# Optimization experiments

Hardware: AMD Instinct MI355X
Metric: run time of the kernel (lower is better)

The kernel has to match this reference:

```python
import jax, jax.numpy as jnp
import numpy as np
from jax import lax

B, C1, C2, OUT, H, W = 8, 256, 128, 256, 64, 64
MID = max(C1, C2)
D = max(MID // 8, 4)

def conv1x1(x, w, b=None):
    # x: [B,C,H,W], w: [O,C]
    y = jnp.einsum('bchw,oc->bohw', x, w)
    if b is not None:
        y = y + b[None, :, None, None]
    return y

def dwconv3x3(x, w, b):
    # depthwise 3x3, padding=1; w: [C,1,3,3]
    y = lax.conv_general_dilated(x, w, (1, 1), 'SAME',
                                 dimension_numbers=('NCHW', 'OIHW', 'NCHW'),
                                 feature_group_count=x.shape[1])
    return y + b[None, :, None, None]

def setup_inputs() -> dict:
    key = jax.random.key(0)
    ks = jax.random.split(key, 16)
    def w1x1(k, o, i):
        return jax.random.normal(k, (o, i), jnp.float32) * np.sqrt(2.0 / o)
    def wdw(k, c):
        return jax.random.normal(k, (c, 1, 3, 3), jnp.float32) * np.sqrt(2.0 / (9 * c))
    z = lambda c: jnp.zeros((c,), jnp.float32)
    return {
        'x1': jax.random.normal(ks[0], (B, C1, H, W), jnp.float32),
        'x2': jax.random.normal(ks[1], (B, C2, H, W), jnp.float32),
        'conv_r_w': w1x1(ks[2], MID, C1), 'conv_r_b': z(MID),
        'conv_n_w': w1x1(ks[3], MID, C2), 'conv_n_b': z(MID),
        'mlp_w1': w1x1(ks[4], D, MID),
        'mlp_w2': w1x1(ks[5], 2 * MID, D),
        'pq_w': w1x1(ks[6], MID, MID), 'pq_b': z(MID),
        'dq_w': wdw(ks[7], MID), 'dq_b': z(MID),
        'pk_w': w1x1(ks[8], MID, MID), 'pk_b': z(MID),
        'dk_w': wdw(ks[9], MID), 'dk_b': z(MID),
        'pv_w': w1x1(ks[10], MID, MID), 'pv_b': z(MID),
        'dv_w': wdw(ks[11], MID), 'dv_b': z(MID),
        'out_w': w1x1(ks[12], OUT, MID), 'out_b': z(OUT),
        'alpha': jnp.float32(1.0),
        'lambd': jnp.float32(0.5),
        'beta': jnp.float32(0.5),
    }

def reference(x1, x2, conv_r_w, conv_r_b, conv_n_w, conv_n_b, mlp_w1, mlp_w2,
              pq_w, pq_b, dq_w, dq_b, pk_w, pk_b, dk_w, dk_b,
              pv_w, pv_b, dv_w, dv_b, out_w, out_b, alpha, lambd, beta):
    FR = conv1x1(x1, conv_r_w, conv_r_b)          # [B,C,H,W]
    FN = conv1x1(x2, conv_n_w, conv_n_b)          # [B,C,H,W]
    stack = jnp.stack([FR, FN], axis=1)           # [B,2,C,H,W]
    feats_sum = FR + FN
    pooled = feats_sum.mean(axis=(2, 3))          # [B,C] (adaptive avg pool 1x1)
    h = jax.nn.relu(jnp.einsum('bc,dc->bd', pooled, mlp_w1))
    a = jnp.einsum('bd,ed->be', h, mlp_w2).reshape(B, 2, MID)
    attn = jax.nn.softmax(a, axis=1)              # softmax over the 2 branches
    Fw = jnp.einsum('bkchw,bkc->bchw', stack, attn)
    Q = dwconv3x3(conv1x1(Fw, pq_w, pq_b), dq_w, dq_b)
    K = dwconv3x3(conv1x1(Fw, pk_w, pk_b), dk_w, dk_b)
    V = dwconv3x3(conv1x1(Fw, pv_w, pv_b), dv_w, dv_b)
    FQ = jnp.fft.fft2(Q.astype(jnp.float32), axes=(-2, -1))   # complex64 [B,C,H,W]
    FK = jnp.fft.fft2(K.astype(jnp.float32), axes=(-2, -1))
    elem = (FQ * FK).reshape(B, MID, H * W)                    # [B,C,HW]
    FQf = FQ.reshape(B, MID, H * W)
    FKf = FK.reshape(B, MID, H * W)
    attn_matrix = jnp.einsum('bcn,bdn->bcd', FQf, FKf)         # complex [B,C,C]
    attn_w = jax.nn.softmax(jnp.abs(attn_matrix) / alpha, axis=-1)
    attn_wc = attn_w.astype(jnp.complex64)
    F_CFR = jnp.einsum('bcd,bdn->bcn', attn_wc, elem).reshape(B, MID, H, W)
    cfr = jnp.real(jnp.fft.ifft2(F_CFR, axes=(-2, -1))).astype(Q.dtype)
    F_DFR = V - lambd * V * cfr
    freq_out = Q * cfr + F_DFR
    output = beta * freq_out + (1.0 - beta) * Fw
    return conv1x1(output, out_w, out_b)
```

## Files before the change

kernel.cpp:

```cpp
#include <hip/hip_runtime.h>
#include <math.h>

#ifndef M_PI
#define M_PI 3.14159265358979323846
#endif

typedef unsigned int u32;

constexpr int  NB   = 8;
constexpr int  CH   = 256;
constexpr long HW   = 4096;
constexpr long SLOT = (long)NB * CH * HW;
constexpr int  SPLITK = 8;
constexpr long ST   = (long)CH * HW;

__device__ __forceinline__ float rne_hi(float x) {
  unsigned u = __float_as_uint(x);
  unsigned r = (u + 0x7FFFu + ((u >> 16) & 1u)) & 0xFFFF0000u;
  return __uint_as_float(r);
}
__device__ __forceinline__ u32 packf(float x) {
  const float h = rne_hi(x);
  const float l = x - h;
  return (__float_as_uint(h) & 0xFFFF0000u) | (__float_as_uint(l) >> 16);
}
__device__ __forceinline__ float unpackf(u32 u) {
  return __uint_as_float(u & 0xFFFF0000u) + __uint_as_float(u << 16);
}
__device__ __forceinline__ unsigned bfpair(float x, float y) {
  return (__float_as_uint(x) >> 16) | (__float_as_uint(y) & 0xFFFF0000u);
}

typedef short bf16x8 __attribute__((ext_vector_type(8)));
typedef float f32x4  __attribute__((ext_vector_type(4)));

__global__ __launch_bounds__(256)
void cvt_kernel(const float* __restrict__ src, u32* __restrict__ dst, int n4)
{
  const int i = blockIdx.x * 256 + threadIdx.x;
  if (i < n4) {
    const float4 v = ((const float4*)src)[i];
    uint4 o;
    o.x = packf(v.x); o.y = packf(v.y); o.z = packf(v.z); o.w = packf(v.w);
    ((uint4*)dst)[i] = o;
  }
}

template<bool BPACKED, int EPI>
__global__ __launch_bounds__(256)
void gemm_mfma(const u32* __restrict__ A, const void* __restrict__ Bv,
               void* __restrict__ Cv, const float* __restrict__ bias,
               int K, long aStride, long bStride, long cStride,
               const u32* __restrict__ qb, const u32* __restrict__ vb,
               const u32* __restrict__ fwb,
               const float* __restrict__ lambd, const float* __restrict__ beta)
{
  constexpr int N = 4096;
  __shared__ __align__(16) unsigned short sAh[128 * 48];
  __shared__ __align__(16) unsigned short sAl[128 * 48];
  __shared__ __align__(16) unsigned short sBh[128 * 48];
  __shared__ __align__(16) unsigned short sBl[128 * 48];

  const int tid = threadIdx.x;
  const int b   = blockIdx.z;
  const int m0  = blockIdx.y * 128;
  const int n0  = blockIdx.x * 128;
  const u32* Ab = A + (long)b * aStride;

  const int ar = tid >> 1;
  const int ak = (tid & 1) * 16;
  const int aBase = ar * 48 + ak;
  const int bn = tid & 127;
  const int bk = (tid >> 7) * 16;
  const int bBase = bn * 48 + bk;

  const int wv = tid >> 6, lane = tid & 63;
  const int wy = wv >> 1, wx = wv & 1;
  const int quad = lane >> 4, l15 = lane & 15;

  f32x4 acc[4][4];
#pragma unroll
  for (int i = 0; i < 4; ++i)
#pragma unroll
    for (int j = 0; j < 4; ++j) acc[i][j] = (f32x4){0.f, 0.f, 0.f, 0.f};

  u32   ra[16];
  u32   rbu[16];
  float rbf[16];
  {
    const u32* ap = Ab + (long)(m0 + ar) * K + ak;
#pragma unroll
    for (int i = 0; i < 4; ++i) {
      const uint4 t = *(const uint4*)(ap + i * 4);
      ra[4*i] = t.x; ra[4*i+1] = t.y; ra[4*i+2] = t.z; ra[4*i+3] = t.w;
    }
    if (BPACKED) {
      const u32* bp = (const u32*)Bv + (long)b * bStride + (long)bk * N + n0 + bn;
#pragma unroll
      for (int i = 0; i < 16; ++i) rbu[i] = bp[(long)i * N];
    } else {
      const float* bp = (const float*)Bv + (long)b * bStride + (long)bk * N + n0 + bn;
#pragma unroll
      for (int i = 0; i < 16; ++i) rbf[i] = bp[(long)i * N];
    }
  }

  for (int kt = 0; kt < K; kt += 32) {
    {
      u32 hi[8], lo[8];
#pragma unroll
      for (int e = 0; e < 8; ++e) {
        const u32 u0 = ra[2*e], u1 = ra[2*e+1];
        hi[e] = (u0 >> 16) | (u1 & 0xFFFF0000u);
        lo[e] = (u0 & 0xFFFFu) | (u1 << 16);
      }
      *(uint4*)&sAh[aBase]     = make_uint4(hi[0], hi[1], hi[2], hi[3]);
      *(uint4*)&sAh[aBase + 8] = make_uint4(hi[4], hi[5], hi[6], hi[7]);
      *(uint4*)&sAl[aBase]     = make_uint4(lo[0], lo[1], lo[2], lo[3]);
      *(uint4*)&sAl[aBase + 8] = make_uint4(lo[4], lo[5], lo[6], lo[7]);
    }
    if (BPACKED) {
      u32 hi[8], lo[8];
#pragma unroll
      for (int e = 0; e < 8; ++e) {
        const u32 u0 = rbu[2*e], u1 = rbu[2*e+1];
        hi[e] = (u0 >> 16) | (u1 & 0xFFFF0000u);
        lo[e] = (u0 & 0xFFFFu) | (u1 << 16);
      }
      *(uint4*)&sBh[bBase]     = make_uint4(hi[0], hi[1], hi[2], hi[3]);
      *(uint4*)&sBh[bBase + 8] = make_uint4(hi[4], hi[5], hi[6], hi[7]);
      *(uint4*)&sBl[bBase]     = make_uint4(lo[0], lo[1], lo[2], lo[3]);
      *(uint4*)&sBl[bBase + 8] = make_uint4(lo[4], lo[5], lo[6], lo[7]);
    } else {
      float h[16], l[16];
#pragma unroll
      for (int e = 0; e < 16; ++e) { h[e] = rne_hi(rbf[e]); l[e] = rbf[e] - h[e]; }
      *(uint4*)&sBh[bBase]     = make_uint4(bfpair(h[0],h[1]), bfpair(h[2],h[3]),
                                            bfpair(h[4],h[5]), bfpair(h[6],h[7]));
      *(uint4*)&sBh[bBase + 8] = make_uint4(bfpair(h[8],h[9]), bfpair(h[10],h[11]),
                                            bfpair(h[12],h[13]), bfpair(h[14],h[15]));
      *(uint4*)&sBl[bBase]     = make_uint4(bfpair(l[0],l[1]), bfpair(l[2],l[3]),
                                            bfpair(l[4],l[5]), bfpair(l[6],l[7]));
      *(uint4*)&sBl[bBase + 8] = make_uint4(bfpair(l[8],l[9]), bfpair(l[10],l[11]),
                                            bfpair(l[12],l[13]), bfpair(l[14],l[15]));
    }
    __syncthreads();

    if (kt + 32 < K) {
      const u32* ap = Ab + (long)(m0 + ar) * K + kt + 32 + ak;
#pragma unroll
      for (int i = 0; i < 4; ++i) {
        const uint4 t = *(const uint4*)(ap + i * 4);
        ra[4*i] = t.x; ra[4*i+1] = t.y; ra[4*i+2] = t.z; ra[4*i+3] = t.w;
      }
      if (BPACKED) {
        const u32* bp = (const u32*)Bv + (long)b * bStride + (long)(kt + 32 + bk) * N + n0 + bn;
#pragma unroll
        for (int i = 0; i < 16; ++i) rbu[i] = bp[(long)i * N];
      } else {
        const float* bp = (const float*)Bv + (long)b * bStride + (long)(kt + 32 + bk) * N + n0 + bn;
#pragma unroll
        for (int i = 0; i < 16; ++i) rbf[i] = bp[(long)i * N];
      }
    }

    bf16x8 ah[4], al[4];
#pragma unroll
    for (int i = 0; i < 4; ++i) {
      const int idx = (wy * 64 + i * 16 + l15) * 48 + quad * 8;
      ah[i] = *(const bf16x8*)&sAh[idx];
      al[i] = *(const bf16x8*)&sAl[idx];
    }
#pragma unroll
    for (int j = 0; j < 4; ++j) {
      const int idx = (wx * 64 + j * 16 + l15) * 48 + quad * 8;
      const bf16x8 bh = *(const bf16x8*)&sBh[idx];
      const bf16x8 bl = *(const bf16x8*)&sBl[idx];
#pragma unroll
      for (int i = 0; i < 4; ++i) {
        acc[i][j] = __builtin_amdgcn_mfma_f32_16x16x32_bf16(ah[i], bh, acc[i][j], 0, 0, 0);
        acc[i][j] = __builtin_amdgcn_mfma_f32_16x16x32_bf16(ah[i], bl, acc[i][j], 0, 0, 0);
        acc[i][j] = __builtin_amdgcn_mfma_f32_16x16x32_bf16(al[i], bh, acc[i][j], 0, 0, 0);
      }
    }
    __syncthreads();
  }

  if (EPI == 0) {
    float* Cb = (float*)Cv + (long)b * cStride;
#pragma unroll
    for (int i = 0; i < 4; ++i)
#pragma unroll
      for (int r = 0; r < 4; ++r) {
        const int row = m0 + wy * 64 + i * 16 + quad * 4 + r;
        const float bb = bias ? bias[row] : 0.f;
#pragma unroll
        for (int j = 0; j < 4; ++j) {
          const int col = n0 + wx * 64 + j * 16 + l15;
          Cb[(long)row * N + col] = acc[i][j][r] + bb;
        }
      }
  } else if (EPI == 1) {
    u32* Cb = (u32*)Cv + (long)b * cStride;
#pragma unroll
    for (int i = 0; i < 4; ++i)
#pragma unroll
      for (int r = 0; r < 4; ++r) {
        const int row = m0 + wy * 64 + i * 16 + quad * 4 + r;
        const float bb = bias ? bias[row] : 0.f;
#pragma unroll
        for (int j = 0; j < 4; ++j) {
          const int col = n0 + wx * 64 + j * 16 + l15;
          Cb[(long)row * N + col] = packf(acc[i][j][r] + bb);
        }
      }
  } else {
    u32* Cb = (u32*)Cv + (long)b * cStride;
    const float lam = lambd[0], bet = beta[0];
#pragma unroll
    for (int i = 0; i < 4; ++i)
#pragma unroll
      for (int r = 0; r < 4; ++r) {
        const int row = m0 + wy * 64 + i * 16 + quad * 4 + r;
#pragma unroll
        for (int j = 0; j < 4; ++j) {
          const int col = n0 + wx * 64 + j * 16 + l15;
          const long off = (long)row * N + col;
          const long gi  = (long)b * cStride + off;
          const float q = unpackf(qb[gi]);
          const float v = unpackf(vb[gi]);
          const float f = unpackf(fwb[gi]);
          Cb[off] = packf(bet * (acc[i][j][r] * (q - lam * v) + v) + (1.f - bet) * f);
        }
      }
  }
}

__global__ __launch_bounds__(256)
void gemm_logits(const u32* __restrict__ Q, const u32* __restrict__ Kr,
                 float* __restrict__ Lp)
{
  __shared__ __align__(16) unsigned short sAh[128 * 48];
  __shared__ __align__(16) unsigned short sAl[128 * 48];
  __shared__ __align__(16) unsigned short sBh[128 * 48];
  __shared__ __align__(16) unsigned short sBl[128 * 48];

  const int tid = threadIdx.x;
  const int bz  = blockIdx.z;
  const int b   = bz >> 3, sp = bz & 7;
  const int m0  = blockIdx.y * 128;
  const int n0  = blockIdx.x * 128;
  const long k0b = (long)sp * 512;

  const int ar = tid >> 1;
  const int ak = (tid & 1) * 16;
  const int aBase = ar * 48 + ak;

  const int wv = tid >> 6, lane = tid & 63;
  const int wy = wv >> 1, wx = wv & 1;
  const int quad = lane >> 4, l15 = lane & 15;

  f32x4 acc[4][4];
#pragma unroll
  for (int i = 0; i < 4; ++i)
#pragma unroll
    for (int j = 0; j < 4; ++j) acc[i][j] = (f32x4){0.f, 0.f, 0.f, 0.f};

  const u32* Abase = Q  + (long)b * ST + (long)(m0 + ar) * 4096 + k0b + ak;
  const u32* Bbase = Kr + (long)b * ST + (long)(n0 + ar) * 4096 + k0b + ak;

  u32 ra[16], rb[16];
#pragma unroll
  for (int i = 0; i < 4; ++i) {
    uint4 t = *(const uint4*)(Abase + i * 4);
    ra[4*i] = t.x; ra[4*i+1] = t.y; ra[4*i+2] = t.z; ra[4*i+3] = t.w;
    t = *(const uint4*)(Bbase + i * 4);
    rb[4*i] = t.x; rb[4*i+1] = t.y; rb[4*i+2] = t.z; rb[4*i+3] = t.w;
  }

  for (int kt = 0; kt < 512; kt += 32) {
    {
      u32 hi[8], lo[8];
#pragma unroll
      for (int e = 0; e < 8; ++e) {
        const u32 u0 = ra[2*e], u1 = ra[2*e+1];
        hi[e] = (u0 >> 16) | (u1 & 0xFFFF0000u);
        lo[e] = (u0 & 0xFFFFu) | (u1 << 16);
      }
      *(uint4*)&sAh[aBase]     = make_uint4(hi[0], hi[1], hi[2], hi[3]);
      *(uint4*)&sAh[aBase + 8] = make_uint4(hi[4], hi[5], hi[6], hi[7]);
      *(uint4*)&sAl[aBase]     = make_uint4(lo[0], lo[1], lo[2], lo[3]);
      *(uint4*)&sAl[aBase + 8] = make_uint4(lo[4], lo[5], lo[6], lo[7]);
#pragma unroll
      for (int e = 0; e < 8; ++e) {
        const u32 u0 = rb[2*e], u1 = rb[2*e+1];
        hi[e] = (u0 >> 16) | (u1 & 0xFFFF0000u);
        lo[e] = (u0 & 0xFFFFu) | (u1 << 16);
      }
      *(uint4*)&sBh[aBase]     = make_uint4(hi[0], hi[1], hi[2], hi[3]);
      *(uint4*)&sBh[aBase + 8] = make_uint4(hi[4], hi[5], hi[6], hi[7]);
      *(uint4*)&sBl[aBase]     = make_uint4(lo[0], lo[1], lo[2], lo[3]);
      *(uint4*)&sBl[aBase + 8] = make_uint4(lo[4], lo[5], lo[6], lo[7]);
    }
    __syncthreads();

    if (kt + 32 < 512) {
#pragma unroll
      for (int i = 0; i < 4; ++i) {
        uint4 t = *(const uint4*)(Abase + kt + 32 + i * 4);
        ra[4*i] = t.x; ra[4*i+1] = t.y; ra[4*i+2] = t.z; ra[4*i+3] = t.w;
        t = *(const uint4*)(Bbase + kt + 32 + i * 4);
        rb[4*i] = t.x; rb[4*i+1] = t.y; rb[4*i+2] = t.z; rb[4*i+3] = t.w;
      }
    }

    bf16x8 ah[4], al[4];
#pragma unroll
    for (int i = 0; i < 4; ++i) {
      const int idx = (wy * 64 + i * 16 + l15) * 48 + quad * 8;
      ah[i] = *(const bf16x8*)&sAh[idx];
      al[i] = *(const bf16x8*)&sAl[idx];
    }
#pragma unroll
    for (int j = 0; j < 4; ++j) {
      const int idx = (wx * 64 + j * 16 + l15) * 48 + quad * 8;
      const bf16x8 bh = *(const bf16x8*)&sBh[idx];
      const bf16x8 bl = *(const bf16x8*)&sBl[idx];
#pragma unroll
      for (int i = 0; i < 4; ++i) {
        acc[i][j] = __builtin_amdgcn_mfma_f32_16x16x32_bf16(ah[i], bh, acc[i][j], 0, 0, 0);
        acc[i][j] = __builtin_amdgcn_mfma_f32_16x16x32_bf16(ah[i], bl, acc[i][j], 0, 0, 0);
        acc[i][j] = __builtin_amdgcn_mfma_f32_16x16x32_bf16(al[i], bh, acc[i][j], 0, 0, 0);
      }
    }
    __syncthreads();
  }

  float* Lb = Lp + (long)bz * 65536;
#pragma unroll
  for (int i = 0; i < 4; ++i)
#pragma unroll
    for (int r = 0; r < 4; ++r) {
      const int row = m0 + wy * 64 + i * 16 + quad * 4 + r;
#pragma unroll
      for (int j = 0; j < 4; ++j) {
        const int col = n0 + wx * 64 + j * 16 + l15;
        Lb[(long)row * 256 + col] = acc[i][j][r];
      }
    }
}

__global__ __launch_bounds__(256)
void pool_kernel(const u32* __restrict__ FR, const u32* __restrict__ FN,
                 float* __restrict__ pooled)
{
  __shared__ float red[256];
  const int bc = blockIdx.x, tid = threadIdx.x;
  const uint4* a = (const uint4*)(FR + (long)bc * HW);
  const uint4* b = (const uint4*)(FN + (long)bc * HW);
  float s = 0.f;
  for (int v = tid; v < 1024; v += 256) {
    const uint4 x = a[v];
    s += unpackf(x.x) + unpackf(x.y) + unpackf(x.z) + unpackf(x.w);
    const uint4 y = b[v];
    s += unpackf(y.x) + unpackf(y.y) + unpackf(y.z) + unpackf(y.w);
  }
  red[tid] = s; __syncthreads();
  for (int o = 128; o > 0; o >>= 1) {
    if (tid < o) red[tid] += red[tid + o];
    __syncthreads();
  }
  if (tid == 0) pooled[bc] = red[0] * (1.f / 4096.f);
}

__global__ __launch_bounds__(256)
void attn2_kernel(const float* __restrict__ pooled, const float* __restrict__ w1,
                  const float* __restrict__ w2, float* __restrict__ attn2)
{
  __shared__ float ps[256];
  __shared__ float hs[32];
  const int b = blockIdx.x, tid = threadIdx.x;
  ps[tid] = pooled[b * 256 + tid];
  __syncthreads();
  if (tid < 32) {
    float a = 0.f;
    for (int c = 0; c < 256; ++c) a += ps[c] * w1[tid * 256 + c];
    hs[tid] = fmaxf(a, 0.f);
  }
  __syncthreads();
  float a0 = 0.f, a1 = 0.f;
  for (int d = 0; d < 32; ++d) {
    const float h = hs[d];
    a0 += h * w2[tid * 32 + d];
    a1 += h * w2[(256 + tid) * 32 + d];
  }
  const float m  = fmaxf(a0, a1);
  const float e0 = expf(a0 - m), e1 = expf(a1 - m);
  const float inv = 1.f / (e0 + e1);
  attn2[b * 512 + tid]       = e0 * inv;
  attn2[b * 512 + 256 + tid] = e1 * inv;
}

__global__ __launch_bounds__(256)
void fw_kernel(const u32* __restrict__ FR, const u32* __restrict__ FN,
               const float* __restrict__ attn2, u32* __restrict__ FW)
{
  const int b = blockIdx.z, c = blockIdx.y;
  const float a0 = attn2[b * 512 + c];
  const float a1 = attn2[b * 512 + 256 + c];
  const long base4 = ((long)b * 256 + c) * 1024;
  const int i = blockIdx.x * 256 + threadIdx.x;
  const uint4 r = ((const uint4*)FR)[base4 + i];
  const uint4 n = ((const uint4*)FN)[base4 + i];
  uint4 o;
  o.x = packf(a0 * unpackf(r.x) + a1 * unpackf(n.x));
  o.y = packf(a0 * unpackf(r.y) + a1 * unpackf(n.y));
  o.z = packf(a0 * unpackf(r.z) + a1 * unpackf(n.z));
  o.w = packf(a0 * unpackf(r.w) + a1 * unpackf(n.w));
  ((uint4*)FW)[base4 + i] = o;
}

__global__ __launch_bounds__(256)
void dw_kernel(const u32* __restrict__ in, const float* __restrict__ w,
               const float* __restrict__ bias, u32* __restrict__ out,
               u32* __restrict__ out_rev)
{
  __shared__ float img[66][66];
  const int bc = blockIdx.x, tid = threadIdx.x;
  const int c = bc & 255;
  for (int v = tid; v < 66 * 66; v += 256) ((float*)img)[v] = 0.f;
  __syncthreads();
  const uint4* in4 = (const uint4*)(in + (long)bc * HW);
  for (int v = tid; v < 1024; v += 256) {
    const uint4 x = in4[v];
    const int r = v >> 4, c0 = ((v & 15) << 2) + 1;
    img[r + 1][c0 + 0] = unpackf(x.x);
    img[r + 1][c0 + 1] = unpackf(x.y);
    img[r + 1][c0 + 2] = unpackf(x.z);
    img[r + 1][c0 + 3] = unpackf(x.w);
  }
  float wr[9];
#pragma unroll
  for (int j = 0; j < 9; ++j) wr[j] = w[c * 9 + j];
  const float bb = bias[c];
  __syncthreads();
  for (int p = tid; p < 4096; p += 256) {
    const int y = p >> 6, x = p & 63;
    float s = bb;
#pragma unroll
    for (int ky = 0; ky < 3; ++ky)
#pragma unroll
      for (int kx = 0; kx < 3; ++kx)
        s = fmaf(wr[ky * 3 + kx], img[y + ky][x + kx], s);
    const u32 u = packf(s);
    out[(long)bc * HW + p] = u;
    if (out_rev)
      out_rev[(long)bc * HW + (((64 - y) & 63) << 6) + ((64 - x) & 63)] = u;
  }
}

#define SWA(r, c) (((r) << 6) | ((c) ^ (r)))
#define REV6(x)   ((((x) & 3) << 4) | ((x) & 12) | ((x) >> 4))

__device__ __forceinline__ float2 cmul(float2 a, float2 w) {
  return make_float2(a.x * w.x - a.y * w.y, a.x * w.y + a.y * w.x);
}
__device__ __forceinline__ float2 cmulc(float2 a, float2 w) {
  return make_float2(a.x * w.x + a.y * w.y, a.y * w.x - a.x * w.y);
}

__global__ __launch_bounds__(256, 4)
void sconv_kernel(const u32* __restrict__ Qg, const u32* __restrict__ Kg,
                  u32* __restrict__ Sg)
{
  __shared__ float Re[4096];
  __shared__ float Im[4096];
  __shared__ float2 twt[64];
  const int tid = threadIdx.x;
  const long base = (long)blockIdx.x * 4096;
  if (tid < 64) {
    float sn, cs;
    __sincosf(-2.f * (float)M_PI * (float)tid * (1.f / 64.f), &sn, &cs);
    twt[tid] = make_float2(cs, sn);
  }
  const uint4* Q4 = (const uint4*)(Qg + base);
  const uint4* K4 = (const uint4*)(Kg + base);
#pragma unroll
  for (int i = 0; i < 4; ++i) {
    const int v = tid + 256 * i;
    const uint4 q = Q4[v], k = K4[v];
    const int r = v >> 4, w = v & 15;
    const int R  = REV6(r);
    const int cb = ((w & 3) << 2) | (w >> 2);
    Re[SWA(R, cb)]      = unpackf(q.x);  Im[SWA(R, cb)]      = unpackf(k.x);
    Re[SWA(R, cb + 16)] = unpackf(q.y);  Im[SWA(R, cb + 16)] = unpackf(k.y);
    Re[SWA(R, cb + 32)] = unpackf(q.z);  Im[SWA(R, cb + 32)] = unpackf(k.z);
    Re[SWA(R, cb + 48)] = unpackf(q.w);  Im[SWA(R, cb + 48)] = unpackf(k.w);
  }
  __syncthreads();

  const int lane = tid & 63;
  const int kb   = tid >> 6;

  for (int pass = 0; pass < 2; ++pass) {
    for (int s = 0; s < 3; ++s) {
      const int h  = 1 << (2 * s);
      const int us = 16 >> (2 * s);
#pragma unroll
      for (int q = 0; q < 4; ++q) {
        const int k = kb + 4 * q;
        const int j = k & (h - 1);
        const int g = k >> (2 * s);
        const int bse = g * 4 * h + j;
        const int p0 = bse, p1 = bse + h, p2 = bse + 2 * h, p3 = bse + 3 * h;
        const int a0 = pass ? SWA(p0, lane) : SWA(lane, p0);
        const int a1 = pass ? SWA(p1, lane) : SWA(lane, p1);
        const int a2 = pass ? SWA(p2, lane) : SWA(lane, p2);
        const int a3 = pass ? SWA(p3, lane) : SWA(lane, p3);
        float2 x0 = make_float2(Re[a0], Im[a0]);
        float2 x1 = make_float2(Re[a1], Im[a1]);
        float2 x2 = make_float2(Re[a2], Im[a2]);
        float2 x3 = make_float2(Re[a3], Im[a3]);
        const int e = j * us;
        x1 = cmul(x1, twt[e & 63]);
        x2 = cmul(x2, twt[(2 * e) & 63]);
        x3 = cmul(x3, twt[(3 * e) & 63]);
        const float2 t0 = make_float2(x0.x + x2.x, x0.y + x2.y);
        const float2 t1 = make_float2(x0.x - x2.x, x0.y - x2.y);
        const float2 t2 = make_float2(x1.x + x3.x, x1.y + x3.y);
        const float2 t3 = make_float2(x1.x - x3.x, x1.y - x3.y);
        Re[a0] = t0.x + t2.x;  Im[a0] = t0.y + t2.y;
        Re[a2] = t0.x - t2.x;  Im[a2] = t0.y - t2.y;
        Re[a1] = t1.x + t3.y;  Im[a1] = t1.y - t3.x;
        Re[a3] = t1.x - t3.y;  Im[a3] = t1.y + t3.x;
      }
      __syncthreads();
    }
  }

  float2 pv[16];
#pragma unroll
  for (int i = 0; i < 16; ++i) {
    const int n = tid + 256 * i;
    const int u = n >> 6, vv = n & 63;
    const int u2 = (64 - u) & 63, v2 = (64 - vv) & 63;
    const int az = SWA(u, vv), am = SWA(u2, v2);
    const float zr = Re[az], zi = Im[az];
    const float mr = Re[am], mi = Im[am];
    const float dre = zr * zr - zi * zi - mr * mr + mi * mi;
    const float dim = 2.f * (zr * zi + mr * mi);
    pv[i] = make_float2(0.25f * dim, -0.25f * dre);
  }
  __syncthreads();
#pragma unroll
  for (int i = 0; i < 16; ++i) {
    const int n = tid + 256 * i;
    const int az = SWA(n >> 6, n & 63);
    Re[az] = pv[i].x;
    Im[az] = pv[i].y;
  }
  __syncthreads();

  for (int pass = 0; pass < 2; ++pass) {
    for (int s = 2; s >= 0; --s) {
      const int h  = 1 << (2 * s);
      const int us = 16 >> (2 * s);
#pragma unroll
      for (int q = 0; q < 4; ++q) {
        const int k = kb + 4 * q;
        const int j = k & (h - 1);
        const int g = k >> (2 * s);
        const int bse = g * 4 * h + j;
        const int p0 = bse, p1 = bse + h, p2 = bse + 2 * h, p3 = bse + 3 * h;
        const int a0 = pass ? SWA(lane, p0) : SWA(p0, lane);
        const int a1 = pass ? SWA(lane, p1) : SWA(p1, lane);
        const int a2 = pass ? SWA(lane, p2) : SWA(p2, lane);
        const int a3 = pass ? SWA(lane, p3) : SWA(p3, lane);
        const float2 x0 = make_float2(Re[a0], Im[a0]);
        const float2 x1 = make_float2(Re[a1], Im[a1]);
        const float2 x2 = make_float2(Re[a2], Im[a2]);
        const float2 x3 = make_float2(Re[a3], Im[a3]);
        const float2 t0 = make_float2(x0.x + x2.x, x0.y + x2.y);
        const float2 t1 = make_float2(x0.x - x2.x, x0.y - x2.y);
        const float2 t2 = make_float2(x1.x + x3.x, x1.y + x3.y);
        const float2 t3 = make_float2(x1.x - x3.x, x1.y - x3.y);
        const float2 y0 = make_float2(t0.x + t2.x, t0.y + t2.y);
        float2 y2 = make_float2(t0.x - t2.x, t0.y - t2.y);
        float2 y1 = make_float2(t1.x - t3.y, t1.y + t3.x);
        float2 y3 = make_float2(t1.x + t3.y, t1.y - t3.x);
        const int e = j * us;
        y1 = cmulc(y1, twt[e & 63]);
        y2 = cmulc(y2, twt[(2 * e) & 63]);
        y3 = cmulc(y3, twt[(3 * e) & 63]);
        Re[a0] = y0.x;  Im[a0] = y0.y;
        Re[a1] = y1.x;  Im[a1] = y1.y;
        Re[a2] = y2.x;  Im[a2] = y2.y;
        Re[a3] = y3.x;  Im[a3] = y3.y;
      }
      __syncthreads();
    }
  }

  uint4* S4 = (uint4*)(Sg + base);
#pragma unroll
  for (int i = 0; i < 4; ++i) {
    const int v = tid + 256 * i;
    const int y = v >> 4, w = v & 15;
    const int Rr = REV6(y);
    const int cb = ((w & 3) << 2) | (w >> 2);
    uint4 o;
    o.x = packf(Re[SWA(Rr, cb)]      * (1.f / 4096.f));
    o.y = packf(Re[SWA(Rr, cb + 16)] * (1.f / 4096.f));
    o.z = packf(Re[SWA(Rr, cb + 32)] * (1.f / 4096.f));
    o.w = packf(Re[SWA(Rr, cb + 48)] * (1.f / 4096.f));
    S4[v] = o;
  }
}

__global__ __launch_bounds__(256)
void softmax_kernel(const float* __restrict__ Lp, u32* __restrict__ L,
                    const float* __restrict__ alpha)
{
  __shared__ float red[256];
  const int row = blockIdx.x, tid = threadIdx.x;
  const int b = row >> 8, c = row & 255;
  const float sc = 4096.f / alpha[0];
  float acc = 0.f;
#pragma unroll
  for (int s = 0; s < SPLITK; ++s)
    acc += Lp[((long)(b * SPLITK + s) * 65536) + (long)c * 256 + tid];
  const float v = fabsf(acc) * sc;
  red[tid] = v; __syncthreads();
  for (int o = 128; o > 0; o >>= 1) {
    if (tid < o) red[tid] = fmaxf(red[tid], red[tid + o]);
    __syncthreads();
  }
  const float mx = red[0];
  __syncthreads();
  const float e = expf(v - mx);
  red[tid] = e; __syncthreads();
  for (int o = 128; o > 0; o >>= 1) {
    if (tid < o) red[tid] += red[tid + o];
    __syncthreads();
  }
  L[(long)row * 256 + tid] = packf(e / red[0]);
}

extern "C" void kernel_launch(void* const* d_in, const int* in_sizes, int n_in,
                              void* d_out, int out_size, void* d_ws, size_t ws_size,
                              hipStream_t stream)
{
  const float* x1       = (const float*)d_in[0];
  const float* x2       = (const float*)d_in[1];
  const float* conv_r_w = (const float*)d_in[2];
  const float* conv_r_b = (const float*)d_in[3];
  const float* conv_n_w = (const float*)d_in[4];
  const float* conv_n_b = (const float*)d_in[5];
  const float* mlp_w1   = (const float*)d_in[6];
  const float* mlp_w2   = (const float*)d_in[7];
  const float* pq_w     = (const float*)d_in[8];
  const float* pq_b     = (const float*)d_in[9];
  const float* dq_w     = (const float*)d_in[10];
  const float* dq_b     = (const float*)d_in[11];
  const float* pk_w     = (const float*)d_in[12];
  const float* pk_b     = (const float*)d_in[13];
  const float* dk_w     = (const float*)d_in[14];
  const float* dk_b     = (const float*)d_in[15];
  const float* pv_w     = (const float*)d_in[16];
  const float* pv_b     = (const float*)d_in[17];
  const float* dv_w     = (const float*)d_in[18];
  const float* dv_b     = (const float*)d_in[19];
  const float* out_w    = (const float*)d_in[20];
  const float* out_b    = (const float*)d_in[21];
  const float* alpha    = (const float*)d_in[22];
  const float* lambd    = (const float*)d_in[23];
  const float* beta     = (const float*)d_in[24];

  u32* s = (u32*)d_ws;
  u32* S0 = s;
  u32* S1 = s + SLOT;
  u32* S2 = s + 2 * SLOT;
  u32* S3 = s + 3 * SLOT;
  u32* S4 = s + 4 * SLOT;
  u32* S5 = s + 5 * SLOT;
  float* Lp     = (float*)(s + 6 * SLOT);
  u32*   Lb     = (u32*)(Lp + (long)8 * SPLITK * 65536);
  float* pooled = (float*)(Lb + (long)8 * 65536);
  float* attn2  = pooled + 2048;
  u32*   wR     = (u32*)(attn2 + 4096);
  u32*   wN     = wR + 65536;
  u32*   wQ     = wN + 32768;
  u32*   wK     = wQ + 65536;
  u32*   wV     = wK + 65536;
  u32*   wO     = wV + 65536;

  const size_t needed =
      (size_t)(6 * SLOT + (long)8 * SPLITK * 65536 + 8L * 65536 + 2048 + 4096
               + 65536 * 5 + 32768) * 4;
  if (ws_size < needed) return;

  const long ST2 = (long)128 * HW;
  const long STL = (long)256 * 256;
  const dim3 gBig(32, 2, 8);

  cvt_kernel<<<64, 256, 0, stream>>>(conv_r_w, wR, 16384);
  cvt_kernel<<<32, 256, 0, stream>>>(conv_n_w, wN, 8192);
  cvt_kernel<<<64, 256, 0, stream>>>(pq_w, wQ, 16384);
  cvt_kernel<<<64, 256, 0, stream>>>(pk_w, wK, 16384);
  cvt_kernel<<<64, 256, 0, stream>>>(pv_w, wV, 16384);
  cvt_kernel<<<64, 256, 0, stream>>>(out_w, wO, 16384);

  gemm_mfma<false, 1><<<gBig, 256, 0, stream>>>(wR, x1, S0, conv_r_b,
      256, 0L, ST, ST, nullptr, nullptr, nullptr, nullptr, nullptr);
  gemm_mfma<false, 1><<<gBig, 256, 0, stream>>>(wN, x2, S1, conv_n_b,
      128, 0L, ST2, ST, nullptr, nullptr, nullptr, nullptr, nullptr);

  pool_kernel<<<2048, 256, 0, stream>>>(S0, S1, pooled);
  attn2_kernel<<<8, 256, 0, stream>>>(pooled, mlp_w1, mlp_w2, attn2);
  fw_kernel<<<dim3(4, 256, 8), 256, 0, stream>>>(S0, S1, attn2, S2);

  gemm_mfma<true, 1><<<gBig, 256, 0, stream>>>(wQ, S2, S3, pq_b,
      256, 0L, ST, ST, nullptr, nullptr, nullptr, nullptr, nullptr);
  gemm_mfma<true, 1><<<gBig, 256, 0, stream>>>(wK, S2, S4, pk_b,
      256, 0L, ST, ST, nullptr, nullptr, nullptr, nullptr, nullptr);
  gemm_mfma<true, 1><<<gBig, 256, 0, stream>>>(wV, S2, S5, pv_b,
      256, 0L, ST, ST, nullptr, nullptr, nullptr, nullptr, nullptr);

  dw_kernel<<<2048, 256, 0, stream>>>(S3, dq_w, dq_b, S0, nullptr);
  dw_kernel<<<2048, 256, 0, stream>>>(S4, dk_w, dk_b, S1, S3);
  dw_kernel<<<2048, 256, 0, stream>>>(S5, dv_w, dv_b, S4, nullptr);

  sconv_kernel<<<2048, 256, 0, stream>>>(S0, S1, S5);

  gemm_logits<<<dim3(2, 2, 64), 256, 0, stream>>>(S0, S3, Lp);
  softmax_kernel<<<2048, 256, 0, stream>>>(Lp, Lb, alpha);

  gemm_mfma<true, 2><<<gBig, 256, 0, stream>>>(Lb, S5, S2, nullptr,
      256, STL, ST, ST, S0, S4, S2, lambd, beta);

  gemm_mfma<true, 0><<<gBig, 256, 0, stream>>>(wO, S2, d_out, out_b,
      256, 0L, ST, ST, nullptr, nullptr, nullptr, nullptr, nullptr);
}
```

Before: 451.4 us.

## Pack two channels into one complex inverse FFT in spectral conv kernel

Each block now handles two channels. It runs two forward FFTs, with Q and K packed into the real and imaginary parts, then combines both pointwise spectra into one complex array so that a single inverse FFT yields both real outputs. Shared memory switches from separate Re/Im arrays to interleaved float2. This removes one of four inverse FFTs per channel pair and halves the grid. The cost is more registers (two 16-element float2 arrays) and fewer blocks in flight.

After: 540.5 us. +19.7%, slower.

```diff
diff --git a/kernel.cpp b/kernel.cpp
--- a/kernel.cpp
+++ b/kernel.cpp
@@ -469,39 +469,11 @@
   return make_float2(a.x * w.x + a.y * w.y, a.y * w.x - a.x * w.y);
 }
 
-__global__ __launch_bounds__(256, 4)
-void sconv_kernel(const u32* __restrict__ Qg, const u32* __restrict__ Kg,
-                  u32* __restrict__ Sg)
-{
-  __shared__ float Re[4096];
-  __shared__ float Im[4096];
-  __shared__ float2 twt[64];
-  const int tid = threadIdx.x;
-  const long base = (long)blockIdx.x * 4096;
-  if (tid < 64) {
-    float sn, cs;
-    __sincosf(-2.f * (float)M_PI * (float)tid * (1.f / 64.f), &sn, &cs);
-    twt[tid] = make_float2(cs, sn);
-  }
-  const uint4* Q4 = (const uint4*)(Qg + base);
-  const uint4* K4 = (const uint4*)(Kg + base);
-#pragma unroll
-  for (int i = 0; i < 4; ++i) {
-    const int v = tid + 256 * i;
-    const uint4 q = Q4[v], k = K4[v];
-    const int r = v >> 4, w = v & 15;
-    const int R  = REV6(r);
-    const int cb = ((w & 3) << 2) | (w >> 2);
-    Re[SWA(R, cb)]      = unpackf(q.x);  Im[SWA(R, cb)]      = unpackf(k.x);
-    Re[SWA(R, cb + 16)] = unpackf(q.y);  Im[SWA(R, cb + 16)] = unpackf(k.y);
-    Re[SWA(R, cb + 32)] = unpackf(q.z);  Im[SWA(R, cb + 32)] = unpackf(k.z);
-    Re[SWA(R, cb + 48)] = unpackf(q.w);  Im[SWA(R, cb + 48)] = unpackf(k.w);
-  }
-  __syncthreads();
-
+__device__ __forceinline__ void fft_fwd(float2* __restrict__ Z,
+                                        const float2* __restrict__ twt, int tid)
+{
   const int lane = tid & 63;
   const int kb   = tid >> 6;
-
   for (int pass = 0; pass < 2; ++pass) {
     for (int s = 0; s < 3; ++s) {
       const int h  = 1 << (2 * s);
@@ -517,10 +489,10 @@
         const int a1 = pass ? SWA(p1, lane) : SWA(lane, p1);
         const int a2 = pass ? SWA(p2, lane) : SWA(lane, p2);
         const int a3 = pass ? SWA(p3, lane) : SWA(lane, p3);
-        float2 x0 = make_float2(Re[a0], Im[a0]);
-        float2 x1 = make_float2(Re[a1], Im[a1]);
-        float2 x2 = make_float2(Re[a2], Im[a2]);
-        float2 x3 = make_float2(Re[a3], Im[a3]);
+        float2 x0 = Z[a0];
+        float2 x1 = Z[a1];
+        float2 x2 = Z[a2];
+        float2 x3 = Z[a3];
         const int e = j * us;
         x1 = cmul(x1, twt[e & 63]);
         x2 = cmul(x2, twt[(2 * e) & 63]);
@@ -529,38 +501,21 @@
         const float2 t1 = make_float2(x0.x - x2.x, x0.y - x2.y);
         const float2 t2 = make_float2(x1.x + x3.x, x1.y + x3.y);
         const float2 t3 = make_float2(x1.x - x3.x, x1.y - x3.y);
-        Re[a0] = t0.x + t2.x;  Im[a0] = t0.y + t2.y;
-        Re[a2] = t0.x - t2.x;  Im[a2] = t0.y - t2.y;
-        Re[a1] = t1.x + t3.y;  Im[a1] = t1.y - t3.x;
-        Re[a3] = t1.x - t3.y;  Im[a3] = t1.y + t3.x;
+        Z[a0] = make_float2(t0.x + t2.x, t0.y + t2.y);
+        Z[a2] = make_float2(t0.x - t2.x, t0.y - t2.y);
+        Z[a1] = make_float2(t1.x + t3.y, t1.y - t3.x);
+        Z[a3] = make_float2(t1.x - t3.y, t1.y + t3.x);
       }
       __syncthreads();
     }
   }
-
-  float2 pv[16];
-#pragma unroll
-  for (int i = 0; i < 16; ++i) {
-    const int n = tid + 256 * i;
-    const int u = n >> 6, vv = n & 63;
-    const int u2 = (64 - u) & 63, v2 = (64 - vv) & 63;
-    const int az = SWA(u, vv), am = SWA(u2, v2);
-    const float zr = Re[az], zi = Im[az];
-    const float mr = Re[am], mi = Im[am];
-    const float dre = zr * zr - zi * zi - mr * mr + mi * mi;
-    const float dim = 2.f * (zr * zi + mr * mi);
-    pv[i] = make_float2(0.25f * dim, -0.25f * dre);
-  }
-  __syncthreads();
-#pragma unroll
-  for (int i = 0; i < 16; ++i) {
-    const int n = tid + 256 * i;
-    const int az = SWA(n >> 6, n & 63);
-    Re[az] = pv[i].x;
-    Im[az] = pv[i].y;
-  }
-  __syncthreads();
-
+}
+
+__device__ __forceinline__ void fft_inv(float2* __restrict__ Z,
+                                        const float2* __restrict__ twt, int tid)
+{
+  const int lane = tid & 63;
+  const int kb   = tid >> 6;
   for (int pass = 0; pass < 2; ++pass) {
     for (int s = 2; s >= 0; --s) {
       const int h  = 1 << (2 * s);
@@ -576,10 +531,10 @@
         const int a1 = pass ? SWA(lane, p1) : SWA(p1, lane);
         const int a2 = pass ? SWA(lane, p2) : SWA(p2, lane);
         const int a3 = pass ? SWA(lane, p3) : SWA(p3, lane);
-        const float2 x0 = make_float2(Re[a0], Im[a0]);
-        const float2 x1 = make_float2(Re[a1], Im[a1]);
-        const float2 x2 = make_float2(Re[a2], Im[a2]);
-        const float2 x3 = make_float2(Re[a3], Im[a3]);
+        const float2 x0 = Z[a0];
+        const float2 x1 = Z[a1];
+        const float2 x2 = Z[a2];
+        const float2 x3 = Z[a3];
         const float2 t0 = make_float2(x0.x + x2.x, x0.y + x2.y);
         const float2 t1 = make_float2(x0.x - x2.x, x0.y - x2.y);
         const float2 t2 = make_float2(x1.x + x3.x, x1.y + x3.y);
@@ -592,28 +547,108 @@
         y1 = cmulc(y1, twt[e & 63]);
         y2 = cmulc(y2, twt[(2 * e) & 63]);
         y3 = cmulc(y3, twt[(3 * e) & 63]);
-        Re[a0] = y0.x;  Im[a0] = y0.y;
-        Re[a1] = y1.x;  Im[a1] = y1.y;
-        Re[a2] = y2.x;  Im[a2] = y2.y;
-        Re[a3] = y3.x;  Im[a3] = y3.y;
+        Z[a0] = y0;
+        Z[a1] = y1;
+        Z[a2] = y2;
+        Z[a3] = y3;
       }
       __syncthreads();
     }
   }
-
-  uint4* S4 = (uint4*)(Sg + base);
+}
+
+#define SCONV_LOAD_CH(OFF) do {                                              \
+    const uint4* Q4 = (const uint4*)(Qg + base + (OFF));                     \
+    const uint4* K4 = (const uint4*)(Kg + base + (OFF));                     \
+    _Pragma("unroll")                                                        \
+    for (int i = 0; i < 4; ++i) {                                            \
+      const int v = tid + 256 * i;                                           \
+      const uint4 q = Q4[v], k = K4[v];                                      \
+      const int r = v >> 4, w = v & 15;                                      \
+      const int R  = REV6(r);                                                \
+      const int cb = ((w & 3) << 2) | (w >> 2);                              \
+      Z[SWA(R, cb)]      = make_float2(unpackf(q.x), unpackf(k.x));          \
+      Z[SWA(R, cb + 16)] = make_float2(unpackf(q.y), unpackf(k.y));          \
+      Z[SWA(R, cb + 32)] = make_float2(unpackf(q.z), unpackf(k.z));          \
+      Z[SWA(R, cb + 48)] = make_float2(unpackf(q.w), unpackf(k.w));          \
+    }                                                                        \
+  } while (0)
+
+#define SCONV_POINTWISE(PV) do {                                             \
+    _Pragma("unroll")                                                        \
+    for (int i = 0; i < 16; ++i) {                                           \
+      const int n = tid + 256 * i;                                           \
+      const int u = n >> 6, vv = n & 63;                                     \
+      const int u2 = (64 - u) & 63, v2 = (64 - vv) & 63;                     \
+      const float2 z = Z[SWA(u, vv)];                                        \
+      const float2 m = Z[SWA(u2, v2)];                                       \
+      const float dre = z.x * z.x - z.y * z.y - m.x * m.x + m.y * m.y;       \
+      const float dim = 2.f * (z.x * z.y + m.x * m.y);                       \
+      PV[i] = make_float2(0.25f * dim, -0.25f * dre);                        \
+    }                                                                        \
+  } while (0)
+
+__global__ __launch_bounds__(256, 4)
+void sconv_kernel(const u32* __restrict__ Qg, const u32* __restrict__ Kg,
+                  u32* __restrict__ Sg)
+{
+  __shared__ float2 Z[4096];
+  __shared__ float2 twt[64];
+  const int tid = threadIdx.x;
+  const long base = (long)blockIdx.x * 8192;
+  if (tid < 64) {
+    float sn, cs;
+    __sincosf(-2.f * (float)M_PI * (float)tid * (1.f / 64.f), &sn, &cs);
+    twt[tid] = make_float2(cs, sn);
+  }
+
+  float2 pv0[16], pv1[16];
+
+  SCONV_LOAD_CH(0);
+  __syncthreads();
+  fft_fwd(Z, twt, tid);
+  SCONV_POINTWISE(pv0);
+  __syncthreads();
+
+  SCONV_LOAD_CH(4096);
+  __syncthreads();
+  fft_fwd(Z, twt, tid);
+  SCONV_POINTWISE(pv1);
+  __syncthreads();
+
+#pragma unroll
+  for (int i = 0; i < 16; ++i) {
+    const int n = tid + 256 * i;
+    const int az = SWA(n >> 6, n & 63);
+    Z[az] = make_float2(pv0[i].x - pv1[i].y, pv0[i].y + pv1[i].x);
+  }
+  __syncthreads();
+
+  fft_inv(Z, twt, tid);
+
+  uint4* Sa = (uint4*)(Sg + base);
+  uint4* Sb = (uint4*)(Sg + base + 4096);
 #pragma unroll
   for (int i = 0; i < 4; ++i) {
     const int v = tid + 256 * i;
     const int y = v >> 4, w = v & 15;
     const int Rr = REV6(y);
     const int cb = ((w & 3) << 2) | (w >> 2);
+    const float2 e0 = Z[SWA(Rr, cb)];
+    const float2 e1 = Z[SWA(Rr, cb + 16)];
+    const float2 e2 = Z[SWA(Rr, cb + 32)];
+    const float2 e3 = Z[SWA(Rr, cb + 48)];
     uint4 o;
-    o.x = packf(Re[SWA(Rr, cb)]      * (1.f / 4096.f));
-    o.y = packf(Re[SWA(Rr, cb + 16)] * (1.f / 4096.f));
-    o.z = packf(Re[SWA(Rr, cb + 32)] * (1.f / 4096.f));
-    o.w = packf(Re[SWA(Rr, cb + 48)] * (1.f / 4096.f));
-    S4[v] = o;
+    o.x = packf(e0.x * (1.f / 4096.f));
+    o.y = packf(e1.x * (1.f / 4096.f));
+    o.z = packf(e2.x * (1.f / 4096.f));
+    o.w = packf(e3.x * (1.f / 4096.f));
+    Sa[v] = o;
+    o.x = packf(e0.y * (1.f / 4096.f));
+    o.y = packf(e1.y * (1.f / 4096.f));
+    o.z = packf(e2.y * (1.f / 4096.f));
+    o.w = packf(e3.y * (1.f / 4096.f));
+    Sb[v] = o;
   }
 }
 
@@ -730,7 +765,7 @@
   dw_kernel<<<2048, 256, 0, stream>>>(S4, dk_w, dk_b, S1, S3);
   dw_kernel<<<2048, 256, 0, stream>>>(S5, dv_w, dv_b, S4, nullptr);
 
-  sconv_kernel<<<2048, 256, 0, stream>>>(S0, S1, S5);
+  sconv_kernel<<<1024, 256, 0, stream>>>(S0, S1, S5);
 
   gemm_logits<<<dim3(2, 2, 64), 256, 0, stream>>>(S0, S3, Lp);
   softmax_kernel<<<2048, 256, 0, stream>>>(Lp, Lb, alpha);
```
